# Kernel optimization log

Hardware: AMD Instinct MI355X
Metric: run time of the kernel (lower is better)

## Reference

```python
import jax, jax.numpy as jnp
import numpy as np

D_MODEL = 1024
N_HEADS = 16
HEAD_DIM = D_MODEL // N_HEADS


def setup_inputs() -> dict:
    key = jax.random.key(0)
    k_x, k_wqkv, k_bqkv, k_wout, k_bout = jax.random.split(key, 5)
    s = 1.0 / np.sqrt(D_MODEL)
    return {
        "x": jax.random.normal(k_x, (4, 2048, D_MODEL), dtype=jnp.float32),
        "W_qkv": jax.random.normal(k_wqkv, (D_MODEL, 3 * D_MODEL), dtype=jnp.float32) * s,
        "b_qkv": jax.random.normal(k_bqkv, (3 * D_MODEL,), dtype=jnp.float32) * 0.01,
        "W_out": jax.random.normal(k_wout, (D_MODEL, D_MODEL), dtype=jnp.float32) * s,
        "b_out": jax.random.normal(k_bout, (D_MODEL,), dtype=jnp.float32) * 0.01,
    }


def reference(x, W_qkv, b_qkv, W_out, b_out):
    B, T, D = x.shape
    H, Hd = N_HEADS, HEAD_DIM
    qkv = x @ W_qkv + b_qkv                          # [B,T,3D]
    qkv = qkv.reshape(B, T, 3, H, Hd)
    q, k, v = (qkv[:, :, i].transpose(0, 2, 1, 3) for i in range(3))  # [B,H,T,Hd]
    scale = 1.0 / np.sqrt(Hd)
    attn = jnp.einsum("bhqd,bhkd->bhqk", q, k) * scale  # [B,H,T,T]
    causal = jnp.tril(jnp.ones((T, T), dtype=bool))
    attn = jnp.where(causal, attn, -jnp.inf)
    attn = jax.nn.softmax(attn, axis=-1)
    out = jnp.einsum("bhqk,bhkd->bhqd", attn, v)     # [B,H,T,Hd]
    out = out.transpose(0, 2, 1, 3).reshape(B, T, D)
    return out @ W_out + b_out
```

## Files before the change

kernel.cpp:

```cpp
#include <hip/hip_runtime.h>
#include <hip/hip_bf16.h>
#include <string.h>


typedef unsigned short u16;
typedef unsigned int u32;
typedef __bf16 bf16x8 __attribute__((ext_vector_type(8)));
typedef float f32x4 __attribute__((ext_vector_type(4)));

#define MFMA16(a, b, c) __builtin_amdgcn_mfma_f32_16x16x32_bf16((a), (b), (c), 0, 0, 0)

__device__ __forceinline__ u16 f2bf(float f) {
  unsigned u = __float_as_uint(f);
  u += 0x7fffu + ((u >> 16) & 1u);
  return (u16)(u >> 16);
}

__device__ __forceinline__ u32 pk2bf(float a, float b) {
  __hip_bfloat162 h = __float22bfloat162_rn(make_float2(a, b));
  u32 r;
  memcpy(&r, &h, 4);
  return r;
}

__device__ __forceinline__ void gload_lds16(const void* g, void* l) {
  __builtin_amdgcn_global_load_lds((const __attribute__((address_space(1))) void*)g,
                                   (__attribute__((address_space(3))) void*)l, 16, 0, 0);
}

__global__ __launch_bounds__(256) void cast_x_kernel(const float* __restrict__ x,
                                                     u16* __restrict__ xb) {
  int i = blockIdx.x * 256 + threadIdx.x;
  float4 v = ((const float4*)x)[i];
  ushort4 o;
  o.x = f2bf(v.x); o.y = f2bf(v.y); o.z = f2bf(v.z); o.w = f2bf(v.w);
  ((ushort4*)xb)[i] = o;
}

__global__ __launch_bounds__(256) void tcast_kernel(const float* __restrict__ W,
                                                    u16* __restrict__ Wt, int K, int N) {
  __shared__ float tile[32][33];
  int n0 = blockIdx.x * 32, k0 = blockIdx.y * 32;
  int tx = threadIdx.x & 31, ty = threadIdx.x >> 5;
#pragma unroll
  for (int i = 0; i < 4; i++) {
    int k = ty + i * 8;
    tile[k][tx] = W[(size_t)(k0 + k) * N + n0 + tx];
  }
  __syncthreads();
#pragma unroll
  for (int i = 0; i < 4; i++) {
    int n = ty + i * 8;
    Wt[(size_t)(n0 + n) * K + k0 + tx] = f2bf(tile[tx][n]);
  }
}

__global__ __launch_bounds__(256) void gemm_qkv_kernel(const u16* __restrict__ A,
                                                       const u16* __restrict__ Bt,
                                                       const float* __restrict__ bias,
                                                       u16* __restrict__ QKV) {
  __shared__ u16 As[128 * 32];
  __shared__ u16 Bs[128 * 32];
  const int tid = threadIdx.x, w = tid >> 6, lane = tid & 63;
  const int g = lane >> 4, c = lane & 15;
  const int wr = w >> 1, wc = w & 1;
  const int m0 = blockIdx.y * 128, n0 = blockIdx.x * 128;
  const int r4 = lane >> 2, c4 = lane & 3;

  f32x4 acc[4][4];
#pragma unroll
  for (int i = 0; i < 4; i++)
#pragma unroll
    for (int j = 0; j < 4; j++) acc[i][j] = (f32x4){0.f, 0.f, 0.f, 0.f};

  for (int k0 = 0; k0 < 1024; k0 += 32) {
    __syncthreads();
#pragma unroll
    for (int i = 0; i < 2; i++) {
      int rowb = w * 32 + i * 16;
      gload_lds16(A + (size_t)(m0 + rowb + r4) * 1024 + k0 + c4 * 8,
                  (char*)As + rowb * 64);
      gload_lds16(Bt + (size_t)(n0 + rowb + r4) * 1024 + k0 + c4 * 8,
                  (char*)Bs + rowb * 64);
    }
    __syncthreads();

    bf16x8 af[4], bf[4];
#pragma unroll
    for (int mt = 0; mt < 4; mt++)
      af[mt] = *(const bf16x8*)(As + (wr * 64 + mt * 16 + c) * 32 + g * 8);
#pragma unroll
    for (int nt = 0; nt < 4; nt++)
      bf[nt] = *(const bf16x8*)(Bs + (wc * 64 + nt * 16 + c) * 32 + g * 8);
#pragma unroll
    for (int mt = 0; mt < 4; mt++)
#pragma unroll
      for (int nt = 0; nt < 4; nt++) acc[mt][nt] = MFMA16(af[mt], bf[nt], acc[mt][nt]);
  }

  const float qscale = (n0 < 1024) ? 0.18033688011112042f : 1.0f;
  float bn[4];
#pragma unroll
  for (int nt = 0; nt < 4; nt++) bn[nt] = bias[n0 + wc * 64 + nt * 16 + c];
#pragma unroll
  for (int mt = 0; mt < 4; mt++) {
#pragma unroll
    for (int r = 0; r < 4; r++) {
      int m = m0 + wr * 64 + mt * 16 + g * 4 + r;
      int bb = m >> 11, t = m & 2047;
#pragma unroll
      for (int nt = 0; nt < 4; nt++) {
        int n = n0 + wc * 64 + nt * 16 + c;
        int which = n >> 10, rem = n & 1023, h = rem >> 6, d = rem & 63;
        float v = (acc[mt][nt][r] + bn[nt]) * qscale;
        QKV[(size_t)which * 8388608 + (((size_t)(bb * 16 + h) * 2048 + t) * 64 + d)] = f2bf(v);
      }
    }
  }
}

__global__ __launch_bounds__(256) void vtrans_kernel(const u16* __restrict__ V,
                                                     u16* __restrict__ Vt) {
  __shared__ u16 tile[64][65];
  int bh = blockIdx.y;
  int kt = blockIdx.x;
  int t0 = kt * 64;
  int tx = threadIdx.x & 63, ty = threadIdx.x >> 6;
  const u16* src = V + ((size_t)bh * 2048 + t0) * 64;
#pragma unroll
  for (int i = 0; i < 16; i++) {
    int tr = i * 4 + ty;
    tile[tr][tx] = src[tr * 64 + tx];
  }
  __syncthreads();
  u16* dst = Vt + ((size_t)(bh * 32 + kt)) * 4096;
#pragma unroll
  for (int i = 0; i < 16; i++) {
    int d = i * 4 + ty;
    dst[d * 64 + tx] = tile[tx][d];
  }
}

__global__ __launch_bounds__(256) void attn_kernel(const u16* __restrict__ Q,
                                                   const u16* __restrict__ K,
                                                   const u16* __restrict__ Vt,
                                                   u16* __restrict__ ctx) {
  const int pr = blockIdx.x;
  const int qtA = pr, qtB = 15 - pr;
  const int h = blockIdx.y, b = blockIdx.z;
  const int bh = b * 16 + h;
  const int tid = threadIdx.x, w = tid >> 6, lane = tid & 63;
  const int g = lane >> 4, c = lane & 15;

  const u16* Kg = K + (size_t)bh * 2048 * 64;
  const u16* Vg = Vt + (size_t)bh * 32 * 4096;

  __shared__ u16 Ks[2][64 * 64];
  __shared__ u16 Vs[2][64 * 64];
  __shared__ u32 Pw[4][16 * 32];
  u32* pw = Pw[w];

  const int srow = lane >> 3;
  const int schunk = (lane & 7) ^ (srow & 7);
  const int cx = c & 7;
  const int off0 = ((g ^ cx) * 8);
  const int off1 = (((g ^ cx) ^ 4) * 8);
  const int sw = cx << 2;

  bf16x8 onesf;
#pragma unroll
  for (int i = 0; i < 8; i++) onesf[i] = (__bf16)1.0f;

  const u16* QgA = Q + ((size_t)bh * 2048 + qtA * 128) * 64;
  bf16x8 aq[2][2];
#pragma unroll
  for (int s = 0; s < 2; s++) {
    aq[s][0] = *(const bf16x8*)(QgA + (w * 32 + s * 16 + c) * 64 + g * 8);
    aq[s][1] = *(const bf16x8*)(QgA + (w * 32 + s * 16 + c) * 64 + 32 + g * 8);
  }

#pragma unroll
  for (int i = 0; i < 2; i++) {
    int rbase = w * 16 + i * 8;
    gload_lds16(Kg + (size_t)(rbase + srow) * 64 + schunk * 8, (char*)(Ks[0]) + rbase * 128);
    gload_lds16(Vg + (size_t)(rbase + srow) * 64 + schunk * 8, (char*)(Vs[0]) + rbase * 128);
  }
  __syncthreads();

  f32x4 o[2][4], la[2];
#pragma unroll
  for (int s = 0; s < 2; s++) {
#pragma unroll
    for (int nt = 0; nt < 4; nt++) o[s][nt] = (f32x4){0.f, 0.f, 0.f, 0.f};
    la[s] = (f32x4){0.f, 0.f, 0.f, 0.f};
  }

  const int nA = 2 * qtA + 2;

  auto store_tile = [&](int qbase) {
#pragma unroll
    for (int s = 0; s < 2; s++) {
      float inv = 1.f / la[s][0];
      int q = qbase + w * 32 + s * 16 + c;
      size_t base = ((size_t)(b * 2048 + q)) * 1024 + h * 64;
#pragma unroll
      for (int nt = 0; nt < 4; nt++) {
        u32 lo = pk2bf(o[s][nt][0] * inv, o[s][nt][1] * inv);
        u32 hi = pk2bf(o[s][nt][2] * inv, o[s][nt][3] * inv);
        *(uint2*)(ctx + base + nt * 16 + g * 4) = make_uint2(lo, hi);
      }
    }
  };

  for (int r = 0; r < 34; r++) {
    if (r) __syncthreads();

    if (r < 33) {
      const int ktn = (r + 1 < nA) ? (r + 1) : (r + 1 - nA);
      const int nb = (r + 1) & 1;
      const u16* Kt = Kg + (size_t)ktn * 4096;
      const u16* Vn = Vg + (size_t)ktn * 4096;
#pragma unroll
      for (int i = 0; i < 2; i++) {
        int rbase = w * 16 + i * 8;
        gload_lds16(Kt + (size_t)(rbase + srow) * 64 + schunk * 8,
                    (char*)(Ks[nb]) + rbase * 128);
        gload_lds16(Vn + (size_t)(rbase + srow) * 64 + schunk * 8,
                    (char*)(Vs[nb]) + rbase * 128);
      }
    }

    const bool inA = (r < nA);
    const int kt = inA ? r : (r - nA);
    const int qbase = inA ? qtA * 128 : qtB * 128;
    const int sb0 = qbase + w * 32;
    const int kb = kt * 64;

    if (kb <= sb0 + 31) {
      const bool live0 = (kb <= sb0 + 15);
      const u16* Kb = Ks[r & 1];
      const u16* Vb = Vs[r & 1];

      f32x4 sa[2][4];
#pragma unroll
      for (int nt = 0; nt < 4; nt++) {
        bf16x8 k0 = *(const bf16x8*)(Kb + (nt * 16 + c) * 64 + off0);
        bf16x8 k1 = *(const bf16x8*)(Kb + (nt * 16 + c) * 64 + off1);
#pragma unroll
        for (int s = 0; s < 2; s++) {
          f32x4 z = (f32x4){0.f, 0.f, 0.f, 0.f};
          z = MFMA16(k0, aq[s][0], z);
          z = MFMA16(k1, aq[s][1], z);
          sa[s][nt] = z;
        }
      }

      bf16x8 pB[2][2];
#pragma unroll
      for (int s = 0; s < 2; s++) {
        const bool live = (s == 0) ? live0 : true;
        if (live) {
          const int sbs = sb0 + s * 16;
          const bool domask = (kb + 63 > sbs);
          float pe[4][4];
#pragma unroll
          for (int nt = 0; nt < 4; nt++)
#pragma unroll
            for (int rr = 0; rr < 4; rr++) {
              float t = sa[s][nt][rr];
              if (domask && (kb + nt * 16 + g * 4 + rr) > (sbs + c)) t = -1e30f;
              pe[nt][rr] = __builtin_amdgcn_exp2f(t);
            }
#pragma unroll
          for (int nt = 0; nt < 4; nt++) {
            u32 lo = pk2bf(pe[nt][0], pe[nt][1]);
            u32 hi = pk2bf(pe[nt][2], pe[nt][3]);
            *(uint2*)(pw + c * 32 + ((nt * 8 + g * 2) ^ sw)) = make_uint2(lo, hi);
          }
          pB[s][0] = *(const bf16x8*)(pw + c * 32 + ((g * 4) ^ sw));
          pB[s][1] = *(const bf16x8*)(pw + c * 32 + ((16 + g * 4) ^ sw));
        }
      }

      la[1] = MFMA16(onesf, pB[1][0], la[1]);
      la[1] = MFMA16(onesf, pB[1][1], la[1]);
      if (live0) {
        la[0] = MFMA16(onesf, pB[0][0], la[0]);
        la[0] = MFMA16(onesf, pB[0][1], la[0]);
      }

#pragma unroll
      for (int nt = 0; nt < 4; nt++) {
        bf16x8 v0 = *(const bf16x8*)(Vb + (nt * 16 + c) * 64 + off0);
        bf16x8 v1 = *(const bf16x8*)(Vb + (nt * 16 + c) * 64 + off1);
        o[1][nt] = MFMA16(v0, pB[1][0], o[1][nt]);
        o[1][nt] = MFMA16(v1, pB[1][1], o[1][nt]);
        if (live0) {
          o[0][nt] = MFMA16(v0, pB[0][0], o[0][nt]);
          o[0][nt] = MFMA16(v1, pB[0][1], o[0][nt]);
        }
      }
    }

    if (r == nA - 1) {
      store_tile(qtA * 128);
#pragma unroll
      for (int s = 0; s < 2; s++) {
#pragma unroll
        for (int nt = 0; nt < 4; nt++) o[s][nt] = (f32x4){0.f, 0.f, 0.f, 0.f};
        la[s] = (f32x4){0.f, 0.f, 0.f, 0.f};
      }
      const u16* QgB = Q + ((size_t)bh * 2048 + qtB * 128) * 64;
#pragma unroll
      for (int s = 0; s < 2; s++) {
        aq[s][0] = *(const bf16x8*)(QgB + (w * 32 + s * 16 + c) * 64 + g * 8);
        aq[s][1] = *(const bf16x8*)(QgB + (w * 32 + s * 16 + c) * 64 + 32 + g * 8);
      }
    }
  }

  store_tile(qtB * 128);
}

__global__ __launch_bounds__(256) void gemm_proj_kernel(const u16* __restrict__ A,
                                                        const u16* __restrict__ Bt,
                                                        const float* __restrict__ bias,
                                                        float* __restrict__ out) {
  __shared__ u16 As[128 * 32];
  __shared__ u16 Bs[128 * 32];
  const int tid = threadIdx.x, w = tid >> 6, lane = tid & 63;
  const int g = lane >> 4, c = lane & 15;
  const int wr = w >> 1, wc = w & 1;
  const int m0 = blockIdx.y * 128, n0 = blockIdx.x * 128;
  const int r4 = lane >> 2, c4 = lane & 3;

  f32x4 acc[4][4];
#pragma unroll
  for (int i = 0; i < 4; i++)
#pragma unroll
    for (int j = 0; j < 4; j++) acc[i][j] = (f32x4){0.f, 0.f, 0.f, 0.f};

  for (int k0 = 0; k0 < 1024; k0 += 32) {
    __syncthreads();
#pragma unroll
    for (int i = 0; i < 2; i++) {
      int rowb = w * 32 + i * 16;
      gload_lds16(A + (size_t)(m0 + rowb + r4) * 1024 + k0 + c4 * 8,
                  (char*)As + rowb * 64);
      gload_lds16(Bt + (size_t)(n0 + rowb + r4) * 1024 + k0 + c4 * 8,
                  (char*)Bs + rowb * 64);
    }
    __syncthreads();

    bf16x8 af[4], bf[4];
#pragma unroll
    for (int mt = 0; mt < 4; mt++)
      af[mt] = *(const bf16x8*)(As + (wr * 64 + mt * 16 + c) * 32 + g * 8);
#pragma unroll
    for (int nt = 0; nt < 4; nt++)
      bf[nt] = *(const bf16x8*)(Bs + (wc * 64 + nt * 16 + c) * 32 + g * 8);
#pragma unroll
    for (int mt = 0; mt < 4; mt++)
#pragma unroll
      for (int nt = 0; nt < 4; nt++) acc[mt][nt] = MFMA16(af[mt], bf[nt], acc[mt][nt]);
  }

  float bn[4];
#pragma unroll
  for (int nt = 0; nt < 4; nt++) bn[nt] = bias[n0 + wc * 64 + nt * 16 + c];
#pragma unroll
  for (int mt = 0; mt < 4; mt++)
#pragma unroll
    for (int r = 0; r < 4; r++) {
      int m = m0 + wr * 64 + mt * 16 + g * 4 + r;
#pragma unroll
      for (int nt = 0; nt < 4; nt++) {
        int n = n0 + wc * 64 + nt * 16 + c;
        out[(size_t)m * 1024 + n] = acc[mt][nt][r] + bn[nt];
      }
    }
}

extern "C" void kernel_launch(void* const* d_in, const int* in_sizes, int n_in,
                              void* d_out, int out_size, void* d_ws, size_t ws_size,
                              hipStream_t stream) {
  const float* x = (const float*)d_in[0];
  const float* Wqkv = (const float*)d_in[1];
  const float* bqkv = (const float*)d_in[2];
  const float* Wout = (const float*)d_in[3];
  const float* bout = (const float*)d_in[4];
  float* out = (float*)d_out;

  char* ws = (char*)d_ws;
  u16* xb  = (u16*)(ws);
  u16* wqt = (u16*)(ws + 16777216);
  u16* wot = (u16*)(ws + 23068672);
  u16* Qb  = (u16*)(ws + 25165824);
  u16* Kb  = Qb + 8388608;
  u16* Vb  = Kb + 8388608;
  u16* Vt  = (u16*)(ws + 75497472);
  u16* ctx = (u16*)(ws + 92274688);

  cast_x_kernel<<<8192, 256, 0, stream>>>(x, xb);
  tcast_kernel<<<dim3(96, 32), 256, 0, stream>>>(Wqkv, wqt, 1024, 3072);
  tcast_kernel<<<dim3(32, 32), 256, 0, stream>>>(Wout, wot, 1024, 1024);
  gemm_qkv_kernel<<<dim3(24, 64), 256, 0, stream>>>(xb, wqt, bqkv, Qb);
  vtrans_kernel<<<dim3(32, 64), 256, 0, stream>>>(Vb, Vt);
  attn_kernel<<<dim3(8, 16, 4), 256, 0, stream>>>(Qb, Kb, Vt, ctx);
  gemm_proj_kernel<<<dim3(8, 64), 256, 0, stream>>>(ctx, wot, bout, out);
}
```

Baseline: 273.0 us.

## Shrink attention Q tile to 64 rows and load V fragments directly from global

The attention kernel now handles 64-row query tiles, paired as qt and 31-qt, instead of 128-row tiles. That doubles the grid to 16x16x4 and adds a min-blocks hint of 4 to launch_bounds. V is no longer staged in LDS: each wave reads its V fragments straight from global memory every iteration, which halves LDS use and simplifies masking to the diagonal tile only. In exchange, every wave re-reads K/V tiles from global or cache more often, and there is less Q-side reuse per K/V load.

```diff
diff --git a/kernel.cpp b/kernel.cpp
--- a/kernel.cpp
+++ b/kernel.cpp
@@ -141,12 +141,12 @@
   }
 }
 
-__global__ __launch_bounds__(256) void attn_kernel(const u16* __restrict__ Q,
-                                                   const u16* __restrict__ K,
-                                                   const u16* __restrict__ Vt,
-                                                   u16* __restrict__ ctx) {
+__global__ __launch_bounds__(256, 4) void attn_kernel(const u16* __restrict__ Q,
+                                                      const u16* __restrict__ K,
+                                                      const u16* __restrict__ Vt,
+                                                      u16* __restrict__ ctx) {
   const int pr = blockIdx.x;
-  const int qtA = pr, qtB = 15 - pr;
+  const int qtA = pr, qtB = 31 - pr;
   const int h = blockIdx.y, b = blockIdx.z;
   const int bh = b * 16 + h;
   const int tid = threadIdx.x, w = tid >> 6, lane = tid & 63;
@@ -156,7 +156,6 @@
   const u16* Vg = Vt + (size_t)bh * 32 * 4096;
 
   __shared__ u16 Ks[2][64 * 64];
-  __shared__ u16 Vs[2][64 * 64];
   __shared__ u32 Pw[4][16 * 32];
   u32* pw = Pw[w];
 
@@ -171,155 +170,116 @@
 #pragma unroll
   for (int i = 0; i < 8; i++) onesf[i] = (__bf16)1.0f;
 
-  const u16* QgA = Q + ((size_t)bh * 2048 + qtA * 128) * 64;
-  bf16x8 aq[2][2];
-#pragma unroll
-  for (int s = 0; s < 2; s++) {
-    aq[s][0] = *(const bf16x8*)(QgA + (w * 32 + s * 16 + c) * 64 + g * 8);
-    aq[s][1] = *(const bf16x8*)(QgA + (w * 32 + s * 16 + c) * 64 + 32 + g * 8);
-  }
+  const u16* QgA = Q + ((size_t)bh * 2048 + qtA * 64) * 64;
+  bf16x8 aq0 = *(const bf16x8*)(QgA + (w * 16 + c) * 64 + g * 8);
+  bf16x8 aq1 = *(const bf16x8*)(QgA + (w * 16 + c) * 64 + 32 + g * 8);
 
 #pragma unroll
   for (int i = 0; i < 2; i++) {
     int rbase = w * 16 + i * 8;
     gload_lds16(Kg + (size_t)(rbase + srow) * 64 + schunk * 8, (char*)(Ks[0]) + rbase * 128);
-    gload_lds16(Vg + (size_t)(rbase + srow) * 64 + schunk * 8, (char*)(Vs[0]) + rbase * 128);
   }
   __syncthreads();
 
-  f32x4 o[2][4], la[2];
-#pragma unroll
-  for (int s = 0; s < 2; s++) {
-#pragma unroll
-    for (int nt = 0; nt < 4; nt++) o[s][nt] = (f32x4){0.f, 0.f, 0.f, 0.f};
-    la[s] = (f32x4){0.f, 0.f, 0.f, 0.f};
-  }
-
-  const int nA = 2 * qtA + 2;
+  f32x4 o[4], la;
+#pragma unroll
+  for (int nt = 0; nt < 4; nt++) o[nt] = (f32x4){0.f, 0.f, 0.f, 0.f};
+  la = (f32x4){0.f, 0.f, 0.f, 0.f};
+
+  const int nA = qtA + 1;
 
   auto store_tile = [&](int qbase) {
-#pragma unroll
-    for (int s = 0; s < 2; s++) {
-      float inv = 1.f / la[s][0];
-      int q = qbase + w * 32 + s * 16 + c;
-      size_t base = ((size_t)(b * 2048 + q)) * 1024 + h * 64;
-#pragma unroll
-      for (int nt = 0; nt < 4; nt++) {
-        u32 lo = pk2bf(o[s][nt][0] * inv, o[s][nt][1] * inv);
-        u32 hi = pk2bf(o[s][nt][2] * inv, o[s][nt][3] * inv);
-        *(uint2*)(ctx + base + nt * 16 + g * 4) = make_uint2(lo, hi);
-      }
+    float inv = 1.f / la[0];
+    int q = qbase + w * 16 + c;
+    size_t base = ((size_t)(b * 2048 + q)) * 1024 + h * 64;
+#pragma unroll
+    for (int nt = 0; nt < 4; nt++) {
+      u32 lo = pk2bf(o[nt][0] * inv, o[nt][1] * inv);
+      u32 hi = pk2bf(o[nt][2] * inv, o[nt][3] * inv);
+      *(uint2*)(ctx + base + nt * 16 + g * 4) = make_uint2(lo, hi);
     }
   };
 
-  for (int r = 0; r < 34; r++) {
+  for (int r = 0; r < 33; r++) {
     if (r) __syncthreads();
 
-    if (r < 33) {
+    if (r < 32) {
       const int ktn = (r + 1 < nA) ? (r + 1) : (r + 1 - nA);
       const int nb = (r + 1) & 1;
       const u16* Kt = Kg + (size_t)ktn * 4096;
-      const u16* Vn = Vg + (size_t)ktn * 4096;
 #pragma unroll
       for (int i = 0; i < 2; i++) {
         int rbase = w * 16 + i * 8;
         gload_lds16(Kt + (size_t)(rbase + srow) * 64 + schunk * 8,
                     (char*)(Ks[nb]) + rbase * 128);
-        gload_lds16(Vn + (size_t)(rbase + srow) * 64 + schunk * 8,
-                    (char*)(Vs[nb]) + rbase * 128);
       }
     }
 
     const bool inA = (r < nA);
     const int kt = inA ? r : (r - nA);
-    const int qbase = inA ? qtA * 128 : qtB * 128;
-    const int sb0 = qbase + w * 32;
-    const int kb = kt * 64;
-
-    if (kb <= sb0 + 31) {
-      const bool live0 = (kb <= sb0 + 15);
-      const u16* Kb = Ks[r & 1];
-      const u16* Vb = Vs[r & 1];
-
-      f32x4 sa[2][4];
-#pragma unroll
-      for (int nt = 0; nt < 4; nt++) {
-        bf16x8 k0 = *(const bf16x8*)(Kb + (nt * 16 + c) * 64 + off0);
-        bf16x8 k1 = *(const bf16x8*)(Kb + (nt * 16 + c) * 64 + off1);
-#pragma unroll
-        for (int s = 0; s < 2; s++) {
-          f32x4 z = (f32x4){0.f, 0.f, 0.f, 0.f};
-          z = MFMA16(k0, aq[s][0], z);
-          z = MFMA16(k1, aq[s][1], z);
-          sa[s][nt] = z;
-        }
+    const int qt = inA ? qtA : qtB;
+
+    const u16* vp = Vg + (size_t)kt * 4096;
+    bf16x8 vb0[4], vb1[4];
+#pragma unroll
+    for (int nt = 0; nt < 4; nt++) {
+      vb0[nt] = *(const bf16x8*)(vp + (nt * 16 + c) * 64 + g * 8);
+      vb1[nt] = *(const bf16x8*)(vp + (nt * 16 + c) * 64 + 32 + g * 8);
+    }
+
+    const u16* Kb = Ks[r & 1];
+
+    f32x4 sa[4];
+#pragma unroll
+    for (int nt = 0; nt < 4; nt++) {
+      bf16x8 k0 = *(const bf16x8*)(Kb + (nt * 16 + c) * 64 + off0);
+      bf16x8 k1 = *(const bf16x8*)(Kb + (nt * 16 + c) * 64 + off1);
+      f32x4 z = (f32x4){0.f, 0.f, 0.f, 0.f};
+      z = MFMA16(k0, aq0, z);
+      z = MFMA16(k1, aq1, z);
+      sa[nt] = z;
+    }
+
+    const bool domask = (kt == qt);
+    float pe[4][4];
+#pragma unroll
+    for (int nt = 0; nt < 4; nt++)
+#pragma unroll
+      for (int rr = 0; rr < 4; rr++) {
+        float t = sa[nt][rr];
+        if (domask && (nt * 16 + g * 4 + rr) > (w * 16 + c)) t = -1e30f;
+        pe[nt][rr] = __builtin_amdgcn_exp2f(t);
       }
-
-      bf16x8 pB[2][2];
-#pragma unroll
-      for (int s = 0; s < 2; s++) {
-        const bool live = (s == 0) ? live0 : true;
-        if (live) {
-          const int sbs = sb0 + s * 16;
-          const bool domask = (kb + 63 > sbs);
-          float pe[4][4];
-#pragma unroll
-          for (int nt = 0; nt < 4; nt++)
-#pragma unroll
-            for (int rr = 0; rr < 4; rr++) {
-              float t = sa[s][nt][rr];
-              if (domask && (kb + nt * 16 + g * 4 + rr) > (sbs + c)) t = -1e30f;
-              pe[nt][rr] = __builtin_amdgcn_exp2f(t);
-            }
-#pragma unroll
-          for (int nt = 0; nt < 4; nt++) {
-            u32 lo = pk2bf(pe[nt][0], pe[nt][1]);
-            u32 hi = pk2bf(pe[nt][2], pe[nt][3]);
-            *(uint2*)(pw + c * 32 + ((nt * 8 + g * 2) ^ sw)) = make_uint2(lo, hi);
-          }
-          pB[s][0] = *(const bf16x8*)(pw + c * 32 + ((g * 4) ^ sw));
-          pB[s][1] = *(const bf16x8*)(pw + c * 32 + ((16 + g * 4) ^ sw));
-        }
-      }
-
-      la[1] = MFMA16(onesf, pB[1][0], la[1]);
-      la[1] = MFMA16(onesf, pB[1][1], la[1]);
-      if (live0) {
-        la[0] = MFMA16(onesf, pB[0][0], la[0]);
-        la[0] = MFMA16(onesf, pB[0][1], la[0]);
-      }
-
-#pragma unroll
-      for (int nt = 0; nt < 4; nt++) {
-        bf16x8 v0 = *(const bf16x8*)(Vb + (nt * 16 + c) * 64 + off0);
-        bf16x8 v1 = *(const bf16x8*)(Vb + (nt * 16 + c) * 64 + off1);
-        o[1][nt] = MFMA16(v0, pB[1][0], o[1][nt]);
-        o[1][nt] = MFMA16(v1, pB[1][1], o[1][nt]);
-        if (live0) {
-          o[0][nt] = MFMA16(v0, pB[0][0], o[0][nt]);
-          o[0][nt] = MFMA16(v1, pB[0][1], o[0][nt]);
-        }
-      }
+#pragma unroll
+    for (int nt = 0; nt < 4; nt++) {
+      u32 lo = pk2bf(pe[nt][0], pe[nt][1]);
+      u32 hi = pk2bf(pe[nt][2], pe[nt][3]);
+      *(uint2*)(pw + c * 32 + ((nt * 8 + g * 2) ^ sw)) = make_uint2(lo, hi);
+    }
+    bf16x8 pB0 = *(const bf16x8*)(pw + c * 32 + ((g * 4) ^ sw));
+    bf16x8 pB1 = *(const bf16x8*)(pw + c * 32 + ((16 + g * 4) ^ sw));
+
+    la = MFMA16(onesf, pB0, la);
+    la = MFMA16(onesf, pB1, la);
+
+#pragma unroll
+    for (int nt = 0; nt < 4; nt++) {
+      o[nt] = MFMA16(vb0[nt], pB0, o[nt]);
+      o[nt] = MFMA16(vb1[nt], pB1, o[nt]);
     }
 
     if (r == nA - 1) {
-      store_tile(qtA * 128);
-#pragma unroll
-      for (int s = 0; s < 2; s++) {
-#pragma unroll
-        for (int nt = 0; nt < 4; nt++) o[s][nt] = (f32x4){0.f, 0.f, 0.f, 0.f};
-        la[s] = (f32x4){0.f, 0.f, 0.f, 0.f};
-      }
-      const u16* QgB = Q + ((size_t)bh * 2048 + qtB * 128) * 64;
-#pragma unroll
-      for (int s = 0; s < 2; s++) {
-        aq[s][0] = *(const bf16x8*)(QgB + (w * 32 + s * 16 + c) * 64 + g * 8);
-        aq[s][1] = *(const bf16x8*)(QgB + (w * 32 + s * 16 + c) * 64 + 32 + g * 8);
-      }
-    }
-  }
-
-  store_tile(qtB * 128);
+      store_tile(qtA * 64);
+#pragma unroll
+      for (int nt = 0; nt < 4; nt++) o[nt] = (f32x4){0.f, 0.f, 0.f, 0.f};
+      la = (f32x4){0.f, 0.f, 0.f, 0.f};
+      const u16* QgB = Q + ((size_t)bh * 2048 + qtB * 64) * 64;
+      aq0 = *(const bf16x8*)(QgB + (w * 16 + c) * 64 + g * 8);
+      aq1 = *(const bf16x8*)(QgB + (w * 16 + c) * 64 + 32 + g * 8);
+    }
+  }
+
+  store_tile(qtB * 64);
 }
 
 __global__ __launch_bounds__(256) void gemm_proj_kernel(const u16* __restrict__ A,
@@ -406,6 +366,6 @@
   tcast_kernel<<<dim3(32, 32), 256, 0, stream>>>(Wout, wot, 1024, 1024);
   gemm_qkv_kernel<<<dim3(24, 64), 256, 0, stream>>>(xb, wqt, bqkv, Qb);
   vtrans_kernel<<<dim3(32, 64), 256, 0, stream>>>(Vb, Vt);
-  attn_kernel<<<dim3(8, 16, 4), 256, 0, stream>>>(Qb, Kb, Vt, ctx);
+  attn_kernel<<<dim3(16, 16, 4), 256, 0, stream>>>(Qb, Kb, Vt, ctx);
   gemm_proj_kernel<<<dim3(8, 64), 256, 0, stream>>>(ctx, wot, bout, out);
 }
```

Result: slower. 327.3 us (+19.9%).
